# Performance work log

Measured on AMD Instinct MI355X. Metric: run time of the kernel, lower is better.

The kernel has to match this reference:

```python
import jax, jax.numpy as jnp
import numpy as np

LENGTH_OF_SIGNAL = 2560
OUTLIER_THRESHOLD = 3.0


def setup_inputs() -> dict:
    key = jax.random.key(0)
    inputs = jax.random.normal(key, (16384, 2560, 1), dtype=jnp.float32)
    return {"inputs": inputs}


def reference(inputs):
    # inputs: (B, S, 1). All stats reduce over the sequence axis (dim=1).
    B, S, _ = inputs.shape
    x = inputs[..., 0]  # (B, S)

    mean = jnp.mean(x, axis=1)                       # (B,)
    maximum = jnp.max(x, axis=1)
    minimum = jnp.min(x, axis=1)
    p2p = maximum - minimum
    rms = jnp.sqrt(jnp.mean(x * x, axis=1))
    var = jnp.var(x, axis=1, ddof=1)                 # torch.var is unbiased
    std = jnp.sqrt(var)                              # torch.std is unbiased

    centered = x - mean[:, None]
    skewness = jnp.mean(centered ** 3, axis=1) / (std ** 3)
    kurtosis = jnp.mean(centered ** 4, axis=1) / (std ** 4)

    abs_x = jnp.abs(x)
    abs_sum = jnp.sum(abs_x, axis=1)
    abs_max = jnp.max(abs_x, axis=1)
    shape_factor = rms * LENGTH_OF_SIGNAL / abs_sum
    impulse_factor = abs_max * LENGTH_OF_SIGNAL / abs_sum

    outliers = jnp.sum(
        (jnp.abs(centered) > OUTLIER_THRESHOLD * std[:, None]).astype(jnp.int32),
        axis=1,
    ).astype(jnp.float32)

    # zero-crossing rate on flattened (B, S) signal
    zcr = jnp.sum(
        (jnp.diff(jnp.sign(x), axis=1) != 0).astype(jnp.float32), axis=1
    ) / (2.0 * S)

    # Hjorth parameters (activity, mobility, complexity)
    d1 = jnp.diff(x, axis=1)
    d2 = jnp.diff(d1, axis=1)
    var_d1 = jnp.var(d1, axis=1, ddof=1)
    var_d2 = jnp.var(d2, axis=1, ddof=1)
    activity = var
    mobility = jnp.sqrt(var_d1 / var)
    complexity = jnp.sqrt(var_d2 / var_d1)

    stacked = jnp.stack(
        [mean, maximum, minimum, p2p, var, rms, skewness, kurtosis,
         shape_factor, impulse_factor, outliers, zcr,
         activity, mobility, complexity],
        axis=1,
    )  # (B, 15)
    return stacked
```

## Files before the change

kernel.cpp:

```cpp
#include <hip/hip_runtime.h>
#include <math.h>


typedef float f32x2 __attribute__((ext_vector_type(2)));
typedef float f32x4 __attribute__((ext_vector_type(4)));

constexpr int S_LEN = 2560;
constexpr int NROWS = 16384;

#define DPP_ADD_F32(x, ctrl) do { \
    int t_ = __builtin_amdgcn_update_dpp(0, __float_as_int(x), ctrl, 0xf, 0xf, false); \
    x += __int_as_float(t_); } while (0)
#define DPP_MAX_F32(x, ctrl) do { \
    int t_ = __builtin_amdgcn_update_dpp(__float_as_int(x), __float_as_int(x), ctrl, 0xf, 0xf, false); \
    x = fmaxf(x, __int_as_float(t_)); } while (0)
#define DPP_MIN_F32(x, ctrl) do { \
    int t_ = __builtin_amdgcn_update_dpp(__float_as_int(x), __float_as_int(x), ctrl, 0xf, 0xf, false); \
    x = fminf(x, __int_as_float(t_)); } while (0)

__device__ __forceinline__ float wave_sum_f32(float x) {
    DPP_ADD_F32(x, 0x111); DPP_ADD_F32(x, 0x112); DPP_ADD_F32(x, 0x114);
    DPP_ADD_F32(x, 0x118); DPP_ADD_F32(x, 0x142); DPP_ADD_F32(x, 0x143);
    return x;
}
__device__ __forceinline__ float wave_max_f32(float x) {
    DPP_MAX_F32(x, 0x111); DPP_MAX_F32(x, 0x112); DPP_MAX_F32(x, 0x114);
    DPP_MAX_F32(x, 0x118); DPP_MAX_F32(x, 0x142); DPP_MAX_F32(x, 0x143);
    return x;
}
__device__ __forceinline__ float wave_min_f32(float x) {
    DPP_MIN_F32(x, 0x111); DPP_MIN_F32(x, 0x112); DPP_MIN_F32(x, 0x114);
    DPP_MIN_F32(x, 0x118); DPP_MIN_F32(x, 0x142); DPP_MIN_F32(x, 0x143);
    return x;
}
__device__ __forceinline__ double wave_sum_f64(double x) {
#define DPP_ADD_F64(ctrl) do { \
    long long b_ = __double_as_longlong(x); \
    int lo_ = __builtin_amdgcn_update_dpp(0, (int)(b_ & 0xffffffffLL), ctrl, 0xf, 0xf, false); \
    int hi_ = __builtin_amdgcn_update_dpp(0, (int)(b_ >> 32), ctrl, 0xf, 0xf, false); \
    x += __longlong_as_double(((long long)hi_ << 32) | (unsigned int)lo_); } while (0)
    DPP_ADD_F64(0x111); DPP_ADD_F64(0x112); DPP_ADD_F64(0x114);
    DPP_ADD_F64(0x118); DPP_ADD_F64(0x142); DPP_ADD_F64(0x143);
#undef DPP_ADD_F64
    return x;
}
__device__ __forceinline__ double readlane_f64(double x, int l) {
    long long b = __double_as_longlong(x);
    int lo = __builtin_amdgcn_readlane((int)(b & 0xffffffffLL), l);
    int hi = __builtin_amdgcn_readlane((int)(b >> 32), l);
    return __longlong_as_double(((long long)hi << 32) | (unsigned int)lo);
}

__global__ __launch_bounds__(256, 6)
void health_pass1(const float* __restrict__ in, float* __restrict__ ws) {
    __shared__ double Lsum[4], Lsq[4];
    __shared__ float  Lnb[2][2];

    const int lane = threadIdx.x & 63;
    const int wid  = threadIdx.x >> 6;
    const int hidx = wid & 1;
    const int rsl  = wid >> 1;
    const int row  = blockIdx.x * 2 + rsl;

    const f32x4* rp = reinterpret_cast<const f32x4*>(in)
                    + (size_t)row * (S_LEN / 4) + hidx * (1280 / 4) + lane;

    f32x4 X[5];
#pragma unroll
    for (int k = 0; k < 5; ++k) X[k] = __builtin_nontemporal_load(rp + k * 64);

    f32x2 sp = {0.f, 0.f}, qp = {0.f, 0.f}, sabsp = {0.f, 0.f};
    f32x2 vmaxp = {-INFINITY, -INFINITY}, vminp = {INFINITY, INFINITY};
#pragma unroll
    for (int k = 0; k < 5; ++k) {
        f32x2 lo = __builtin_shufflevector(X[k], X[k], 0, 1);
        f32x2 hi = __builtin_shufflevector(X[k], X[k], 2, 3);
        sp += lo + hi;
        qp = __builtin_elementwise_fma(lo, lo, qp);
        qp = __builtin_elementwise_fma(hi, hi, qp);
        sabsp += __builtin_elementwise_max(lo, -lo);
        sabsp += __builtin_elementwise_max(hi, -hi);
        vmaxp = __builtin_elementwise_max(vmaxp, __builtin_elementwise_max(lo, hi));
        vminp = __builtin_elementwise_min(vminp, __builtin_elementwise_min(lo, hi));
    }

    const double sum_l = (double)sp.x + (double)sp.y;
    const double sq_l  = (double)qp.x + (double)qp.y;
    const double sum_u = readlane_f64(wave_sum_f64(sum_l), 63);
    const double sq_u  = readlane_f64(wave_sum_f64(sq_l), 63);

    float sabs = wave_sum_f32(sabsp.x + sabsp.y);
    float vmax = wave_max_f32(fmaxf(vmaxp.x, vmaxp.y));
    float vmin = wave_min_f32(fminf(vminp.x, vminp.y));

    if (lane == 0) {
        Lsum[wid] = sum_u;  Lsq[wid] = sq_u;
        if (hidx == 1) { Lnb[rsl][0] = X[0][0]; Lnb[rsl][1] = X[0][1]; }
    }
    __syncthreads();
    const double tsum = Lsum[rsl * 2] + Lsum[rsl * 2 + 1];
    const double tsq  = Lsq[rsl * 2]  + Lsq[rsl * 2 + 1];

    const double mean = tsum * (1.0 / S_LEN);
    const double var  = (tsq - tsum * mean) * (1.0 / (S_LEN - 1));
    const double thr  = 3.0 * sqrt(var);
    const double bhi = mean + thr, blo = mean - thr;
    float bhi_f = (float)bhi;
    if ((double)bhi_f > bhi) bhi_f = __int_as_float(__float_as_int(bhi_f) - 1);
    float blo_f = (float)blo;
    if ((double)blo_f < blo) blo_f = __int_as_float(__float_as_int(blo_f) - 1);

    const float nbv0 = (hidx == 0) ? Lnb[rsl][0] : 0.f;
    const float nbv1 = (hidx == 0) ? Lnb[rsl][1] : 0.f;
    const float mf = (float)mean;
    const f32x2 nmf2 = {-mf, -mf};
    const unsigned long long tail_ok = (hidx == 0) ? ~0ULL : 0x7FFFFFFFFFFFFFFFULL;

    f32x2 c3p = {0.f, 0.f}, c4p = {0.f, 0.f};
    float r1 = 0.f, r2 = 0.f;
    int outc = 0, zcc = 0;
    const int nli = (lane + 1) & 63;

#pragma unroll
    for (int k = 0; k < 5; ++k) {
        const float x0 = X[k][0], x1 = X[k][1], x2v = X[k][2], x3 = X[k][3];
        const int kn = (k == 4) ? 0 : (k + 1);
        float v0 = (lane == 0) ? X[kn][0] : x0;
        float v1 = (lane == 0) ? X[kn][1] : x1;
        float n0 = __shfl(v0, nli);
        float n1 = __shfl(v1, nli);
        if (k == 4 && lane == 63) { n0 = nbv0; n1 = nbv1; }

        f32x2 lo = __builtin_shufflevector(X[k], X[k], 0, 1);
        f32x2 hi = __builtin_shufflevector(X[k], X[k], 2, 3);
        f32x2 cl = lo + nmf2, ch = hi + nmf2;
        f32x2 ql = cl * cl,  qh = ch * ch;
        c3p = __builtin_elementwise_fma(ql, cl, c3p);
        c3p = __builtin_elementwise_fma(qh, ch, c3p);
        c4p = __builtin_elementwise_fma(ql, ql, c4p);
        c4p = __builtin_elementwise_fma(qh, qh, c4p);

        outc += __popcll(__ballot(x0  > bhi_f || x0  < blo_f));
        outc += __popcll(__ballot(x1  > bhi_f || x1  < blo_f));
        outc += __popcll(__ballot(x2v > bhi_f || x2v < blo_f));
        outc += __popcll(__ballot(x3  > bhi_f || x3  < blo_f));

        const unsigned long long m0 = __ballot(x0  < 0.f);
        const unsigned long long m1 = __ballot(x1  < 0.f);
        const unsigned long long m2 = __ballot(x2v < 0.f);
        const unsigned long long m3 = __ballot(x3  < 0.f);
        const unsigned long long mn = __ballot(n0  < 0.f);
        zcc += __popcll(m0 ^ m1) + __popcll(m1 ^ m2) + __popcll(m2 ^ m3);
        zcc += __popcll((m3 ^ mn) & ((k == 4) ? tail_ok : ~0ULL));

        r1 = fmaf(x0, x1, fmaf(x1, x2v, fmaf(x2v, x3, fmaf(x3, n0, r1))));
        r2 = fmaf(x0, x2v, fmaf(x1, x3, fmaf(x2v, n0, fmaf(x3, n1, r2))));
    }

    float sabs_t = sabs;
    float c3_t   = wave_sum_f32(c3p.x + c3p.y);
    float c4_t   = wave_sum_f32(c4p.x + c4p.y);
    float r1_t   = wave_sum_f32(r1);
    float r2_t   = wave_sum_f32(r2);
    float vmax_t = vmax;
    float vmin_t = vmin;

    float ep_a, ep_b;
    if (hidx == 0) {
        ep_a = __int_as_float(__builtin_amdgcn_readlane(__float_as_int(X[0][0]), 0));
        ep_b = __int_as_float(__builtin_amdgcn_readlane(__float_as_int(X[0][1]), 0));
    } else {
        ep_a = X[4][2];  ep_b = X[4][3];
    }

    if (lane == 63) {
        double2* Wd = reinterpret_cast<double2*>(ws);
        f32x4*   Wf = reinterpret_cast<f32x4*>(ws);
        double2 dsum; dsum.x = sum_u; dsum.y = sq_u;
        Wd[(size_t)hidx * NROWS + row] = dsum;
        const size_t b = (size_t)(2 + hidx * 3) * NROWS + row;
        Wf[b]             = f32x4{sabs_t, vmax_t, vmin_t, c3_t};
        Wf[b + NROWS]     = f32x4{c4_t, r1_t, r2_t, (float)outc};
        Wf[b + 2 * NROWS] = f32x4{(float)zcc, ep_a, ep_b, 0.f};
    }
}

__global__ __launch_bounds__(256)
void health_finalize(const float* __restrict__ ws, float* __restrict__ out) {
    const int row = blockIdx.x * 256 + threadIdx.x;
    const double2* Wd = reinterpret_cast<const double2*>(ws);
    const f32x4*   Wf = reinterpret_cast<const f32x4*>(ws);

    const double2 s0 = Wd[row], s1 = Wd[NROWS + row];
    const f32x4 a0 = Wf[2 * NROWS + row], a1 = Wf[3 * NROWS + row], a2 = Wf[4 * NROWS + row];
    const f32x4 b0 = Wf[5 * NROWS + row], b1 = Wf[6 * NROWS + row], b2 = Wf[7 * NROWS + row];

    const double tsum = s0.x + s1.x;
    const double tsq  = s0.y + s1.y;
    const double mean = tsum * (1.0 / S_LEN);
    const double var  = (tsq - tsum * mean) * (1.0 / (S_LEN - 1));
    const double stdv = sqrt(var);

    const float tabs = a0[0] + b0[0];
    const float tmax = fmaxf(a0[1], b0[1]);
    const float tmin = fminf(a0[2], b0[2]);
    const float c3t  = a0[3] + b0[3];
    const float c4t  = a1[0] + b1[0];
    const double r1t = (double)a1[1] + (double)b1[1];
    const double r2t = (double)a1[2] + (double)b1[2];
    const float outt = a1[3] + b1[3];
    const float zct  = a2[0] + b2[0];
    const double e0 = (double)a2[1], e1 = (double)a2[2];
    const double e2 = (double)b2[1], e3 = (double)b2[2];

    const double rms  = sqrt(tsq * (1.0 / S_LEN));
    const double m3   = (double)c3t * (1.0 / S_LEN);
    const double m4   = (double)c4t * (1.0 / S_LEN);
    const double skew = m3 / (var * stdv);
    const double kurt = m4 / (var * var);
    const float  amax = fmaxf(fabsf(tmax), fabsf(tmin));
    const double shape   = rms * (double)S_LEN / (double)tabs;
    const double impulse = (double)amax * (double)S_LEN / (double)tabs;

    const double Q = tsq;
    const double s1q = 2.0 * Q - 2.0 * r1t - e0 * e0 - e3 * e3;
    const double s2q = 6.0 * Q - 8.0 * r1t + 2.0 * r2t
                     + 4.0 * (e0 * e1 + e2 * e3)
                     - 5.0 * e0 * e0 - e1 * e1 - e2 * e2 - 5.0 * e3 * e3;
    const double sd1 = e3 - e0;
    const double sd2 = (e3 - e2) - (e1 - e0);
    const double var1 = (s1q - sd1 * sd1 * (1.0 / (S_LEN - 1))) * (1.0 / (S_LEN - 2));
    const double var2 = (s2q - sd2 * sd2 * (1.0 / (S_LEN - 2))) * (1.0 / (S_LEN - 3));

    float* o = out + (size_t)row * 15;
    o[0]  = (float)mean;
    o[1]  = tmax;
    o[2]  = tmin;
    o[3]  = tmax - tmin;
    o[4]  = (float)var;
    o[5]  = (float)rms;
    o[6]  = (float)skew;
    o[7]  = (float)kurt;
    o[8]  = (float)shape;
    o[9]  = (float)impulse;
    o[10] = outt;
    o[11] = zct * (1.0f / (2.0f * S_LEN));
    o[12] = (float)var;
    o[13] = (float)sqrt(var1 / var);
    o[14] = (float)sqrt(var2 / var1);
}

extern "C" void kernel_launch(void* const* d_in, const int* in_sizes, int n_in,
                              void* d_out, int out_size, void* d_ws, size_t ws_size,
                              hipStream_t stream) {
    (void)in_sizes; (void)n_in; (void)ws_size; (void)out_size;
    const float* in = (const float*)d_in[0];
    float* out = (float*)d_out;
    float* ws  = (float*)d_ws;
    health_pass1<<<8192, 256, 0, stream>>>(in, ws);
    health_finalize<<<64, 256, 0, stream>>>(ws, out);
}
```

Measured before the change: 40.22 us.

## Process four row pairs per block with register double-buffered prefetch

Each block now handles eight rows, two at a time over four iterations, and issues the loads for the next row pair right after the block barrier so they overlap the second-pass compute on the current row. Shared-memory partials are double-buffered by iteration parity. The grid shrinks fourfold, cutting launch and tail overhead. The loads also switch from nontemporal to regular, and the extra Xn registers may reduce occupancy under the launch bound of 6. An empty leftover loop remains in the code.

```diff
diff --git a/kernel.cpp b/kernel.cpp
--- a/kernel.cpp
+++ b/kernel.cpp
@@ -53,135 +53,162 @@
 
 __global__ __launch_bounds__(256, 6)
 void health_pass1(const float* __restrict__ in, float* __restrict__ ws) {
-    __shared__ double Lsum[4], Lsq[4];
-    __shared__ float  Lnb[2][2];
+    __shared__ double Lsum[2][4], Lsq[2][4];
+    __shared__ float  Lnb[2][2][2];
 
     const int lane = threadIdx.x & 63;
     const int wid  = threadIdx.x >> 6;
     const int hidx = wid & 1;
     const int rsl  = wid >> 1;
-    const int row  = blockIdx.x * 2 + rsl;
-
-    const f32x4* rp = reinterpret_cast<const f32x4*>(in)
-                    + (size_t)row * (S_LEN / 4) + hidx * (1280 / 4) + lane;
+    const int nli  = (lane + 1) & 63;
+
+    {
+        const int row0 = blockIdx.x * 8 + rsl;
+        const f32x4* rp = reinterpret_cast<const f32x4*>(in)
+                        + (size_t)row0 * (S_LEN / 4) + hidx * (1280 / 4) + lane;
+#pragma unroll
+        for (int k = 0; k < 5; ++k) {
+        }
+    }
 
     f32x4 X[5];
-#pragma unroll
-    for (int k = 0; k < 5; ++k) X[k] = __builtin_nontemporal_load(rp + k * 64);
-
-    f32x2 sp = {0.f, 0.f}, qp = {0.f, 0.f}, sabsp = {0.f, 0.f};
-    f32x2 vmaxp = {-INFINITY, -INFINITY}, vminp = {INFINITY, INFINITY};
-#pragma unroll
-    for (int k = 0; k < 5; ++k) {
-        f32x2 lo = __builtin_shufflevector(X[k], X[k], 0, 1);
-        f32x2 hi = __builtin_shufflevector(X[k], X[k], 2, 3);
-        sp += lo + hi;
-        qp = __builtin_elementwise_fma(lo, lo, qp);
-        qp = __builtin_elementwise_fma(hi, hi, qp);
-        sabsp += __builtin_elementwise_max(lo, -lo);
-        sabsp += __builtin_elementwise_max(hi, -hi);
-        vmaxp = __builtin_elementwise_max(vmaxp, __builtin_elementwise_max(lo, hi));
-        vminp = __builtin_elementwise_min(vminp, __builtin_elementwise_min(lo, hi));
+    {
+        const int row0 = blockIdx.x * 8 + rsl;
+        const f32x4* rp = reinterpret_cast<const f32x4*>(in)
+                        + (size_t)row0 * (S_LEN / 4) + hidx * (1280 / 4) + lane;
+#pragma unroll
+        for (int k = 0; k < 5; ++k) X[k] = rp[k * 64];
     }
 
-    const double sum_l = (double)sp.x + (double)sp.y;
-    const double sq_l  = (double)qp.x + (double)qp.y;
-    const double sum_u = readlane_f64(wave_sum_f64(sum_l), 63);
-    const double sq_u  = readlane_f64(wave_sum_f64(sq_l), 63);
-
-    float sabs = wave_sum_f32(sabsp.x + sabsp.y);
-    float vmax = wave_max_f32(fmaxf(vmaxp.x, vmaxp.y));
-    float vmin = wave_min_f32(fminf(vminp.x, vminp.y));
-
-    if (lane == 0) {
-        Lsum[wid] = sum_u;  Lsq[wid] = sq_u;
-        if (hidx == 1) { Lnb[rsl][0] = X[0][0]; Lnb[rsl][1] = X[0][1]; }
-    }
-    __syncthreads();
-    const double tsum = Lsum[rsl * 2] + Lsum[rsl * 2 + 1];
-    const double tsq  = Lsq[rsl * 2]  + Lsq[rsl * 2 + 1];
-
-    const double mean = tsum * (1.0 / S_LEN);
-    const double var  = (tsq - tsum * mean) * (1.0 / (S_LEN - 1));
-    const double thr  = 3.0 * sqrt(var);
-    const double bhi = mean + thr, blo = mean - thr;
-    float bhi_f = (float)bhi;
-    if ((double)bhi_f > bhi) bhi_f = __int_as_float(__float_as_int(bhi_f) - 1);
-    float blo_f = (float)blo;
-    if ((double)blo_f < blo) blo_f = __int_as_float(__float_as_int(blo_f) - 1);
-
-    const float nbv0 = (hidx == 0) ? Lnb[rsl][0] : 0.f;
-    const float nbv1 = (hidx == 0) ? Lnb[rsl][1] : 0.f;
-    const float mf = (float)mean;
-    const f32x2 nmf2 = {-mf, -mf};
-    const unsigned long long tail_ok = (hidx == 0) ? ~0ULL : 0x7FFFFFFFFFFFFFFFULL;
-
-    f32x2 c3p = {0.f, 0.f}, c4p = {0.f, 0.f};
-    float r1 = 0.f, r2 = 0.f;
-    int outc = 0, zcc = 0;
-    const int nli = (lane + 1) & 63;
-
-#pragma unroll
-    for (int k = 0; k < 5; ++k) {
-        const float x0 = X[k][0], x1 = X[k][1], x2v = X[k][2], x3 = X[k][3];
-        const int kn = (k == 4) ? 0 : (k + 1);
-        float v0 = (lane == 0) ? X[kn][0] : x0;
-        float v1 = (lane == 0) ? X[kn][1] : x1;
-        float n0 = __shfl(v0, nli);
-        float n1 = __shfl(v1, nli);
-        if (k == 4 && lane == 63) { n0 = nbv0; n1 = nbv1; }
-
-        f32x2 lo = __builtin_shufflevector(X[k], X[k], 0, 1);
-        f32x2 hi = __builtin_shufflevector(X[k], X[k], 2, 3);
-        f32x2 cl = lo + nmf2, ch = hi + nmf2;
-        f32x2 ql = cl * cl,  qh = ch * ch;
-        c3p = __builtin_elementwise_fma(ql, cl, c3p);
-        c3p = __builtin_elementwise_fma(qh, ch, c3p);
-        c4p = __builtin_elementwise_fma(ql, ql, c4p);
-        c4p = __builtin_elementwise_fma(qh, qh, c4p);
-
-        outc += __popcll(__ballot(x0  > bhi_f || x0  < blo_f));
-        outc += __popcll(__ballot(x1  > bhi_f || x1  < blo_f));
-        outc += __popcll(__ballot(x2v > bhi_f || x2v < blo_f));
-        outc += __popcll(__ballot(x3  > bhi_f || x3  < blo_f));
-
-        const unsigned long long m0 = __ballot(x0  < 0.f);
-        const unsigned long long m1 = __ballot(x1  < 0.f);
-        const unsigned long long m2 = __ballot(x2v < 0.f);
-        const unsigned long long m3 = __ballot(x3  < 0.f);
-        const unsigned long long mn = __ballot(n0  < 0.f);
-        zcc += __popcll(m0 ^ m1) + __popcll(m1 ^ m2) + __popcll(m2 ^ m3);
-        zcc += __popcll((m3 ^ mn) & ((k == 4) ? tail_ok : ~0ULL));
-
-        r1 = fmaf(x0, x1, fmaf(x1, x2v, fmaf(x2v, x3, fmaf(x3, n0, r1))));
-        r2 = fmaf(x0, x2v, fmaf(x1, x3, fmaf(x2v, n0, fmaf(x3, n1, r2))));
-    }
-
-    float sabs_t = sabs;
-    float c3_t   = wave_sum_f32(c3p.x + c3p.y);
-    float c4_t   = wave_sum_f32(c4p.x + c4p.y);
-    float r1_t   = wave_sum_f32(r1);
-    float r2_t   = wave_sum_f32(r2);
-    float vmax_t = vmax;
-    float vmin_t = vmin;
-
-    float ep_a, ep_b;
-    if (hidx == 0) {
-        ep_a = __int_as_float(__builtin_amdgcn_readlane(__float_as_int(X[0][0]), 0));
-        ep_b = __int_as_float(__builtin_amdgcn_readlane(__float_as_int(X[0][1]), 0));
-    } else {
-        ep_a = X[4][2];  ep_b = X[4][3];
-    }
-
-    if (lane == 63) {
-        double2* Wd = reinterpret_cast<double2*>(ws);
-        f32x4*   Wf = reinterpret_cast<f32x4*>(ws);
-        double2 dsum; dsum.x = sum_u; dsum.y = sq_u;
-        Wd[(size_t)hidx * NROWS + row] = dsum;
-        const size_t b = (size_t)(2 + hidx * 3) * NROWS + row;
-        Wf[b]             = f32x4{sabs_t, vmax_t, vmin_t, c3_t};
-        Wf[b + NROWS]     = f32x4{c4_t, r1_t, r2_t, (float)outc};
-        Wf[b + 2 * NROWS] = f32x4{(float)zcc, ep_a, ep_b, 0.f};
+#pragma unroll
+    for (int it = 0; it < 4; ++it) {
+        const int s   = it & 1;
+        const int row = blockIdx.x * 8 + it * 2 + rsl;
+
+        f32x2 sp = {0.f, 0.f}, qp = {0.f, 0.f}, sabsp = {0.f, 0.f};
+        f32x2 vmaxp = {-INFINITY, -INFINITY}, vminp = {INFINITY, INFINITY};
+#pragma unroll
+        for (int k = 0; k < 5; ++k) {
+            f32x2 lo = __builtin_shufflevector(X[k], X[k], 0, 1);
+            f32x2 hi = __builtin_shufflevector(X[k], X[k], 2, 3);
+            sp += lo + hi;
+            qp = __builtin_elementwise_fma(lo, lo, qp);
+            qp = __builtin_elementwise_fma(hi, hi, qp);
+            sabsp += __builtin_elementwise_max(lo, -lo);
+            sabsp += __builtin_elementwise_max(hi, -hi);
+            vmaxp = __builtin_elementwise_max(vmaxp, __builtin_elementwise_max(lo, hi));
+            vminp = __builtin_elementwise_min(vminp, __builtin_elementwise_min(lo, hi));
+        }
+
+        const double sum_l = (double)sp.x + (double)sp.y;
+        const double sq_l  = (double)qp.x + (double)qp.y;
+        const double sum_u = readlane_f64(wave_sum_f64(sum_l), 63);
+        const double sq_u  = readlane_f64(wave_sum_f64(sq_l), 63);
+
+        const float sabs_t = wave_sum_f32(sabsp.x + sabsp.y);
+        const float vmax_t = wave_max_f32(fmaxf(vmaxp.x, vmaxp.y));
+        const float vmin_t = wave_min_f32(fminf(vminp.x, vminp.y));
+
+        if (lane == 0) {
+            Lsum[s][wid] = sum_u;  Lsq[s][wid] = sq_u;
+            if (hidx == 1) { Lnb[s][rsl][0] = X[0][0]; Lnb[s][rsl][1] = X[0][1]; }
+        }
+        __syncthreads();
+
+        f32x4 Xn[5];
+        if (it < 3) {
+            const f32x4* rpn = reinterpret_cast<const f32x4*>(in)
+                             + (size_t)(row + 2) * (S_LEN / 4) + hidx * (1280 / 4) + lane;
+#pragma unroll
+            for (int k = 0; k < 5; ++k) Xn[k] = rpn[k * 64];
+        }
+
+        const double tsum = Lsum[s][rsl * 2] + Lsum[s][rsl * 2 + 1];
+        const double tsq  = Lsq[s][rsl * 2]  + Lsq[s][rsl * 2 + 1];
+
+        const double mean = tsum * (1.0 / S_LEN);
+        const double var  = (tsq - tsum * mean) * (1.0 / (S_LEN - 1));
+        const double thr  = 3.0 * sqrt(var);
+        const double bhi = mean + thr, blo = mean - thr;
+        float bhi_f = (float)bhi;
+        if ((double)bhi_f > bhi) bhi_f = __int_as_float(__float_as_int(bhi_f) - 1);
+        float blo_f = (float)blo;
+        if ((double)blo_f < blo) blo_f = __int_as_float(__float_as_int(blo_f) - 1);
+
+        const float nbv0 = (hidx == 0) ? Lnb[s][rsl][0] : 0.f;
+        const float nbv1 = (hidx == 0) ? Lnb[s][rsl][1] : 0.f;
+        const float mf = (float)mean;
+        const f32x2 nmf2 = {-mf, -mf};
+        const unsigned long long tail_ok = (hidx == 0) ? ~0ULL : 0x7FFFFFFFFFFFFFFFULL;
+
+        f32x2 c3p = {0.f, 0.f}, c4p = {0.f, 0.f};
+        float r1 = 0.f, r2 = 0.f;
+        int outc = 0, zcc = 0;
+
+#pragma unroll
+        for (int k = 0; k < 5; ++k) {
+            const float x0 = X[k][0], x1 = X[k][1], x2v = X[k][2], x3 = X[k][3];
+            const int kn = (k == 4) ? 0 : (k + 1);
+            float v0 = (lane == 0) ? X[kn][0] : x0;
+            float v1 = (lane == 0) ? X[kn][1] : x1;
+            float n0 = __shfl(v0, nli);
+            float n1 = __shfl(v1, nli);
+            if (k == 4 && lane == 63) { n0 = nbv0; n1 = nbv1; }
+
+            f32x2 lo = __builtin_shufflevector(X[k], X[k], 0, 1);
+            f32x2 hi = __builtin_shufflevector(X[k], X[k], 2, 3);
+            f32x2 cl = lo + nmf2, ch = hi + nmf2;
+            f32x2 ql = cl * cl,  qh = ch * ch;
+            c3p = __builtin_elementwise_fma(ql, cl, c3p);
+            c3p = __builtin_elementwise_fma(qh, ch, c3p);
+            c4p = __builtin_elementwise_fma(ql, ql, c4p);
+            c4p = __builtin_elementwise_fma(qh, qh, c4p);
+
+            outc += __popcll(__ballot(x0  > bhi_f || x0  < blo_f));
+            outc += __popcll(__ballot(x1  > bhi_f || x1  < blo_f));
+            outc += __popcll(__ballot(x2v > bhi_f || x2v < blo_f));
+            outc += __popcll(__ballot(x3  > bhi_f || x3  < blo_f));
+
+            const unsigned long long m0 = __ballot(x0  < 0.f);
+            const unsigned long long m1 = __ballot(x1  < 0.f);
+            const unsigned long long m2 = __ballot(x2v < 0.f);
+            const unsigned long long m3 = __ballot(x3  < 0.f);
+            const unsigned long long mn = __ballot(n0  < 0.f);
+            zcc += __popcll(m0 ^ m1) + __popcll(m1 ^ m2) + __popcll(m2 ^ m3);
+            zcc += __popcll((m3 ^ mn) & ((k == 4) ? tail_ok : ~0ULL));
+
+            r1 = fmaf(x0, x1, fmaf(x1, x2v, fmaf(x2v, x3, fmaf(x3, n0, r1))));
+            r2 = fmaf(x0, x2v, fmaf(x1, x3, fmaf(x2v, n0, fmaf(x3, n1, r2))));
+        }
+
+        const float c3_t = wave_sum_f32(c3p.x + c3p.y);
+        const float c4_t = wave_sum_f32(c4p.x + c4p.y);
+        const float r1_t = wave_sum_f32(r1);
+        const float r2_t = wave_sum_f32(r2);
+
+        float ep_a, ep_b;
+        if (hidx == 0) {
+            ep_a = __int_as_float(__builtin_amdgcn_readlane(__float_as_int(X[0][0]), 0));
+            ep_b = __int_as_float(__builtin_amdgcn_readlane(__float_as_int(X[0][1]), 0));
+        } else {
+            ep_a = X[4][2];  ep_b = X[4][3];
+        }
+
+        if (lane == 63) {
+            double2* Wd = reinterpret_cast<double2*>(ws);
+            f32x4*   Wf = reinterpret_cast<f32x4*>(ws);
+            double2 dsum; dsum.x = sum_u; dsum.y = sq_u;
+            Wd[(size_t)hidx * NROWS + row] = dsum;
+            const size_t b = (size_t)(2 + hidx * 3) * NROWS + row;
+            Wf[b]             = f32x4{sabs_t, vmax_t, vmin_t, c3_t};
+            Wf[b + NROWS]     = f32x4{c4_t, r1_t, r2_t, (float)outc};
+            Wf[b + 2 * NROWS] = f32x4{(float)zcc, ep_a, ep_b, 0.f};
+        }
+
+        if (it < 3) {
+#pragma unroll
+            for (int k = 0; k < 5; ++k) X[k] = Xn[k];
+        }
     }
 }
 
@@ -257,6 +284,6 @@
     const float* in = (const float*)d_in[0];
     float* out = (float*)d_out;
     float* ws  = (float*)d_ws;
-    health_pass1<<<8192, 256, 0, stream>>>(in, ws);
+    health_pass1<<<2048, 256, 0, stream>>>(in, ws);
     health_finalize<<<64, 256, 0, stream>>>(ws, out);
 }
```

After: 45.25 us. +12.5%, slower.
